# Kernel optimization log

Measured on AMD Instinct MI355X. Metric: run time of the kernel, lower is better.

The kernel has to match this reference:

```python
import jax, jax.numpy as jnp
import numpy as np

ALPHA = 1.0
EPS = 1e-09
N_PATCH = 128


def _triplet_loss(xp, xn, alpha, eps):
    # xp, xn: [B, N, D], assumed L2-normalized rows
    n = xp.shape[1]
    p_dist = 2.0 - 2.0 * jnp.einsum('bnd,bmd->bnm', xp, xp)   # [B,N,N]
    pn_dist = 2.0 - 2.0 * jnp.einsum('bnd,bmd->bnm', xp, xn)  # [B,N,N]
    # ppn_dist[b,i,j,k] = alpha + p_dist[b,i,j] - pn_dist[b,i,k]
    ppn = alpha + p_dist[:, :, :, None] - pn_dist[:, :, None, :]  # [B,N,N,N]
    mask = ppn <= 0
    pos = jnp.where(mask, 0.0, ppn)
    num = jnp.sum(pos, axis=-1)                                # [B,N,N]
    den = n - jnp.sum(mask, axis=-1).astype(pos.dtype) + eps   # [B,N,N]
    return jnp.mean(num / den)


def setup_inputs() -> dict:
    key = jax.random.key(0)
    latent = jax.random.normal(key, (8192, 512), dtype=jnp.float32)
    return {"latent": latent}


def reference(latent):
    bsz = latent.shape[0] // (2 * N_PATCH)
    latent = latent / jnp.linalg.norm(latent, axis=-1, keepdims=True)
    latent = latent.reshape(bsz, 2, N_PATCH, -1)
    t_latent, c_latent = latent[:, 0], latent[:, 1]
    loss = _triplet_loss(t_latent, c_latent, ALPHA, EPS) + _triplet_loss(c_latent, t_latent, ALPHA, EPS)
    return loss
```

## Files before the change

kernel.cpp:

```cpp
#include <hip/hip_runtime.h>
#include <hip/hip_bf16.h>

constexpr int   D      = 512;
constexpr float ALPHA  = 1.0f;
constexpr float EPS    = 1e-9f;
constexpr float INV_CNT = 1.0f / (32.0f * 128.0f * 128.0f);

constexpr size_t NRM_OFF  = 0;
constexpr size_t PART_OFF = 8388608;

typedef short bf16x8 __attribute__((ext_vector_type(8)));
typedef float f32x4  __attribute__((ext_vector_type(4)));

__device__ __forceinline__ short f2bf(float f) {
    unsigned u = __builtin_bit_cast(unsigned, f);
    unsigned r = (u + 0x7FFFu + ((u >> 16) & 1u)) >> 16;
    return (short)r;
}


__global__ __launch_bounds__(256) void k_normalize(const float* __restrict__ in,
                                                   short* __restrict__ nrm2) {
    const int wid  = threadIdx.x >> 6;
    const int lane = threadIdx.x & 63;
    const int p    = blockIdx.x;
    const int r    = (p & 7) * 1024 + (p >> 3) * 4 + wid;
    const int b    = r >> 8;
    const int row  = r & 255;
    const float4* src = (const float4*)(in + (size_t)r * D);
    float4 x0 = src[2 * lane];
    float4 x1 = src[2 * lane + 1];
    float ss = x0.x*x0.x + x0.y*x0.y + x0.z*x0.z + x0.w*x0.w
             + x1.x*x1.x + x1.y*x1.y + x1.z*x1.z + x1.w*x1.w;
    #pragma unroll
    for (int o = 32; o > 0; o >>= 1) ss += __shfl_xor(ss, o, 64);
    const float inv = rsqrtf(ss);
    bf16x8 v;
    v[0] = f2bf(x0.x * inv); v[1] = f2bf(x0.y * inv);
    v[2] = f2bf(x0.z * inv); v[3] = f2bf(x0.w * inv);
    v[4] = f2bf(x1.x * inv); v[5] = f2bf(x1.y * inv);
    v[6] = f2bf(x1.z * inv); v[7] = f2bf(x1.w * inv);
    const int ks   = lane >> 2;
    const int slot = ((lane & 3) + (row >> 1)) & 3;
    char* dst = (char*)nrm2 + ((((size_t)b * 16 + ks) * 256 + row) * 64 + slot * 16);
    *(bf16x8*)dst = v;
}

constexpr int PSTR = 260;

__global__ __launch_bounds__(1024, 4) void k_fused(const short* __restrict__ nrm2,
                                                   float* __restrict__ part) {
    __shared__ __align__(16) char smem[33408];

    const int p     = blockIdx.x;
    const int slot  = p >> 3;
    const int b     = (p & 7) * 4 + (slot & 3);
    const int chunk = slot >> 2;
    const int w     = threadIdx.x >> 6;
    const int lane  = threadIdx.x & 63;
    const int fr    = lane & 15;
    const int kg    = lane >> 4;

    const char* batchbase = (const char*)nrm2 + (size_t)b * 16 * 256 * 64;

    const int sigma = (kg + (fr >> 1)) & 3;

    const char* gAt = batchbase + (chunk * 16 + fr) * 64 + sigma * 16;
    const char* gAc = gAt + 128 * 64;
    const char* gB0 = batchbase + (w * 16 + fr) * 64 + sigma * 16;

    f32x4 accT = {0.f,0.f,0.f,0.f};
    f32x4 accC = {0.f,0.f,0.f,0.f};

    #pragma unroll
    for (int s = 0; s < 16; s++) {
        const size_t o = (size_t)s * 16384;
        const bf16x8 at = *(const bf16x8*)(gAt + o);
        const bf16x8 ac = *(const bf16x8*)(gAc + o);
        const bf16x8 b0 = *(const bf16x8*)(gB0 + o);
        accT = __builtin_amdgcn_mfma_f32_16x16x32_bf16(at, b0, accT, 0, 0, 0);
        accC = __builtin_amdgcn_mfma_f32_16x16x32_bf16(ac, b0, accC, 0, 0, 0);
    }

    float* P   = (float*)smem;
    float* red = (float*)&smem[33280];

    {
        const int rw = kg * 4;
        const int cw = w * 16 + fr;
        #pragma unroll
        for (int q = 0; q < 4; q++) P[(rw + q) * PSTR + cw]      = accT[q];
        #pragma unroll
        for (int q = 0; q < 4; q++) P[(16 + rw + q) * PSTR + cw] = accC[q];
    }
    __syncthreads();

    float wacc = 0.f;
    #pragma unroll
    for (int rr = 0; rr < 2; rr++) {
        const int r      = w * 2 + rr;
        const int pd_off = (r < 16) ? 0 : 128;
        const int pn_off = 128 - pd_off;
        float* prow = &P[r * PSTR];

        const float g0 = prow[pd_off + lane];
        const float g1 = prow[pd_off + lane + 64];
        float v0 = prow[pn_off + lane];
        float v1 = prow[pn_off + lane + 64];

        #pragma unroll
        for (int kk = 2; kk <= 128; kk <<= 1) {
            if (kk == 128) {
                const float lo = fminf(v0, v1);
                const float hi = fmaxf(v0, v1);
                v0 = lo; v1 = hi;
            }
            #pragma unroll
            for (int j = (kk == 128 ? 32 : (kk >> 1)); j >= 1; j >>= 1) {
                const float p0 = __shfl_xor(v0, j, 64);
                const float p1 = __shfl_xor(v1, j, 64);
                const bool up0 = (lane & kk) == 0;
                const bool up1 = ((lane + 64) & kk) == 0;
                const bool lower = (lane & j) == 0;
                v0 = (up0 == lower) ? fminf(v0, p0) : fmaxf(v0, p0);
                v1 = (up1 == lower) ? fminf(v1, p1) : fmaxf(v1, p1);
            }
        }

        float inc0 = v0, inc1 = v1;
        #pragma unroll
        for (int o = 1; o < 64; o <<= 1) {
            const float t0 = __shfl_up(inc0, o, 64);
            const float t1 = __shfl_up(inc1, o, 64);
            if (lane >= o) { inc0 += t0; inc1 += t1; }
        }
        const float tot0  = __shfl(inc0, 63, 64);
        const float total = tot0 + __shfl(inc1, 63, 64);

        prow[lane]            = v0;
        prow[64 + lane]       = v1;
        prow[130 + 1 + lane]  = inc0;
        prow[130 + 65 + lane] = tot0 + inc1;
        if (lane == 0) prow[130] = 0.f;

        #pragma unroll
        for (int h = 0; h < 2; h++) {
            const float g   = h ? g1 : g0;
            const float tau = g - 0.5f * ALPHA;
            const float a   = ALPHA - 2.f * g;
            int pos = 0;
            #pragma unroll
            for (int st = 128; st > 0; st >>= 1) {
                const int nidx = pos + st;
                const float sv = prow[nidx - 1];
                pos = ((nidx <= 128) && (sv <= tau)) ? nidx : pos;
            }
            const float cnt = (float)(128 - pos);
            const float pre = prow[130 + pos];
            const float num = cnt * a + 2.f * (total - pre);
            wacc += num / (cnt + EPS);
        }
    }

    #pragma unroll
    for (int o = 32; o > 0; o >>= 1) wacc += __shfl_xor(wacc, o, 64);
    if (lane == 0) red[w] = wacc;
    __syncthreads();
    if (threadIdx.x == 0) {
        float s = 0.f;
        #pragma unroll
        for (int i = 0; i < 16; i++) s += red[i];
        part[p] = s;
    }
}

__global__ __launch_bounds__(256) void k_reduce(const float* __restrict__ part,
                                                float* __restrict__ out) {
    __shared__ float red[4];
    const int w    = threadIdx.x >> 6;
    const int lane = threadIdx.x & 63;
    float s = part[threadIdx.x];
    #pragma unroll
    for (int o = 32; o > 0; o >>= 1) s += __shfl_xor(s, o, 64);
    if (lane == 0) red[w] = s;
    __syncthreads();
    if (threadIdx.x == 0)
        out[0] = (red[0] + red[1] + red[2] + red[3]) * INV_CNT;
}

extern "C" void kernel_launch(void* const* d_in, const int* in_sizes, int n_in,
                              void* d_out, int out_size, void* d_ws, size_t ws_size,
                              hipStream_t stream) {
    const float* latent = (const float*)d_in[0];
    float* out  = (float*)d_out;
    char*  wsb  = (char*)d_ws;
    short* nrm2 = (short*)(wsb + NRM_OFF);
    float* part = (float*)(wsb + PART_OFF);

    hipLaunchKernelGGL(k_normalize, dim3(2048), dim3(256),  0, stream, latent, nrm2);
    hipLaunchKernelGGL(k_fused,     dim3(256),  dim3(1024), 0, stream, nrm2, part);
    hipLaunchKernelGGL(k_reduce,    dim3(1),    dim3(256),  0, stream, part, out);
}
```

Before: 28.08 us.

## Split fused block work by half to double grid size and occupancy

Each fused block now computes only one 16-row Gram tile (either the t or the c half) instead of both, so the grid doubles to 512 blocks and each wave processes a single row in the sort/scan phase. Shared memory per block is halved and launch bounds allow more resident blocks, aiming for better latency hiding on a GPU with many CUs. The B-operand loads are now duplicated across the two halves, adding L2 traffic, and the final reduction is widened to 512 partials.

```diff
diff --git a/kernel.cpp b/kernel.cpp
--- a/kernel.cpp
+++ b/kernel.cpp
@@ -48,14 +48,16 @@
 
 constexpr int PSTR = 260;
 
-__global__ __launch_bounds__(1024, 4) void k_fused(const short* __restrict__ nrm2,
+__global__ __launch_bounds__(1024, 8) void k_fused(const short* __restrict__ nrm2,
                                                    float* __restrict__ part) {
-    __shared__ __align__(16) char smem[33408];
+    __shared__ __align__(16) char smem[16768];
 
     const int p     = blockIdx.x;
     const int slot  = p >> 3;
     const int b     = (p & 7) * 4 + (slot & 3);
-    const int chunk = slot >> 2;
+    const int rem   = slot >> 2;
+    const int chunk = rem & 7;
+    const int half  = rem >> 3;
     const int w     = threadIdx.x >> 6;
     const int lane  = threadIdx.x & 63;
     const int fr    = lane & 15;
@@ -65,101 +67,91 @@
 
     const int sigma = (kg + (fr >> 1)) & 3;
 
-    const char* gAt = batchbase + (chunk * 16 + fr) * 64 + sigma * 16;
-    const char* gAc = gAt + 128 * 64;
-    const char* gB0 = batchbase + (w * 16 + fr) * 64 + sigma * 16;
+    const char* gA = batchbase + (half * 128 + chunk * 16 + fr) * 64 + sigma * 16;
+    const char* gB = batchbase + (w * 16 + fr) * 64 + sigma * 16;
 
-    f32x4 accT = {0.f,0.f,0.f,0.f};
-    f32x4 accC = {0.f,0.f,0.f,0.f};
+    f32x4 acc = {0.f, 0.f, 0.f, 0.f};
 
     #pragma unroll
     for (int s = 0; s < 16; s++) {
         const size_t o = (size_t)s * 16384;
-        const bf16x8 at = *(const bf16x8*)(gAt + o);
-        const bf16x8 ac = *(const bf16x8*)(gAc + o);
-        const bf16x8 b0 = *(const bf16x8*)(gB0 + o);
-        accT = __builtin_amdgcn_mfma_f32_16x16x32_bf16(at, b0, accT, 0, 0, 0);
-        accC = __builtin_amdgcn_mfma_f32_16x16x32_bf16(ac, b0, accC, 0, 0, 0);
+        const bf16x8 a  = *(const bf16x8*)(gA + o);
+        const bf16x8 b0 = *(const bf16x8*)(gB + o);
+        acc = __builtin_amdgcn_mfma_f32_16x16x32_bf16(a, b0, acc, 0, 0, 0);
     }
 
     float* P   = (float*)smem;
-    float* red = (float*)&smem[33280];
+    float* red = (float*)&smem[16640];
 
     {
         const int rw = kg * 4;
         const int cw = w * 16 + fr;
         #pragma unroll
-        for (int q = 0; q < 4; q++) P[(rw + q) * PSTR + cw]      = accT[q];
-        #pragma unroll
-        for (int q = 0; q < 4; q++) P[(16 + rw + q) * PSTR + cw] = accC[q];
+        for (int q = 0; q < 4; q++) P[(rw + q) * PSTR + cw] = acc[q];
     }
     __syncthreads();
 
+    const int pd_off = half ? 128 : 0;
+    const int pn_off = 128 - pd_off;
+    float* prow = &P[w * PSTR];
+
+    const float g0 = prow[pd_off + lane];
+    const float g1 = prow[pd_off + lane + 64];
+    float v0 = prow[pn_off + lane];
+    float v1 = prow[pn_off + lane + 64];
+
+    #pragma unroll
+    for (int kk = 2; kk <= 128; kk <<= 1) {
+        if (kk == 128) {
+            const float lo = fminf(v0, v1);
+            const float hi = fmaxf(v0, v1);
+            v0 = lo; v1 = hi;
+        }
+        #pragma unroll
+        for (int j = (kk == 128 ? 32 : (kk >> 1)); j >= 1; j >>= 1) {
+            const float p0 = __shfl_xor(v0, j, 64);
+            const float p1 = __shfl_xor(v1, j, 64);
+            const bool up0 = (lane & kk) == 0;
+            const bool up1 = ((lane + 64) & kk) == 0;
+            const bool lower = (lane & j) == 0;
+            v0 = (up0 == lower) ? fminf(v0, p0) : fmaxf(v0, p0);
+            v1 = (up1 == lower) ? fminf(v1, p1) : fmaxf(v1, p1);
+        }
+    }
+
+    float inc0 = v0, inc1 = v1;
+    #pragma unroll
+    for (int o = 1; o < 64; o <<= 1) {
+        const float t0 = __shfl_up(inc0, o, 64);
+        const float t1 = __shfl_up(inc1, o, 64);
+        if (lane >= o) { inc0 += t0; inc1 += t1; }
+    }
+    const float tot0  = __shfl(inc0, 63, 64);
+    const float total = tot0 + __shfl(inc1, 63, 64);
+
+    prow[lane]            = v0;
+    prow[64 + lane]       = v1;
+    prow[130 + 1 + lane]  = inc0;
+    prow[130 + 65 + lane] = tot0 + inc1;
+    if (lane == 0) prow[130] = 0.f;
+
     float wacc = 0.f;
     #pragma unroll
-    for (int rr = 0; rr < 2; rr++) {
-        const int r      = w * 2 + rr;
-        const int pd_off = (r < 16) ? 0 : 128;
-        const int pn_off = 128 - pd_off;
-        float* prow = &P[r * PSTR];
-
-        const float g0 = prow[pd_off + lane];
-        const float g1 = prow[pd_off + lane + 64];
-        float v0 = prow[pn_off + lane];
-        float v1 = prow[pn_off + lane + 64];
-
+    for (int h = 0; h < 2; h++) {
+        const float g   = h ? g1 : g0;
+        const float tau = g - 0.5f * ALPHA;
+        const float a   = ALPHA - 2.f * g;
+        int pos = 0;
         #pragma unroll
-        for (int kk = 2; kk <= 128; kk <<= 1) {
-            if (kk == 128) {
-                const float lo = fminf(v0, v1);
-                const float hi = fmaxf(v0, v1);
-                v0 = lo; v1 = hi;
-            }
-            #pragma unroll
-            for (int j = (kk == 128 ? 32 : (kk >> 1)); j >= 1; j >>= 1) {
-                const float p0 = __shfl_xor(v0, j, 64);
-                const float p1 = __shfl_xor(v1, j, 64);
-                const bool up0 = (lane & kk) == 0;
-                const bool up1 = ((lane + 64) & kk) == 0;
-                const bool lower = (lane & j) == 0;
-                v0 = (up0 == lower) ? fminf(v0, p0) : fmaxf(v0, p0);
-                v1 = (up1 == lower) ? fminf(v1, p1) : fmaxf(v1, p1);
-            }
+        for (int st = 128; st > 0; st >>= 1) {
+            const int nidx = pos + st;
+            const float sv = prow[nidx - 1];
+            pos = ((nidx <= 128) && (sv <= tau)) ? nidx : pos;
         }
-
-        float inc0 = v0, inc1 = v1;
-        #pragma unroll
-        for (int o = 1; o < 64; o <<= 1) {
-            const float t0 = __shfl_up(inc0, o, 64);
-            const float t1 = __shfl_up(inc1, o, 64);
-            if (lane >= o) { inc0 += t0; inc1 += t1; }
-        }
-        const float tot0  = __shfl(inc0, 63, 64);
-        const float total = tot0 + __shfl(inc1, 63, 64);
-
-        prow[lane]            = v0;
-        prow[64 + lane]       = v1;
-        prow[130 + 1 + lane]  = inc0;
-        prow[130 + 65 + lane] = tot0 + inc1;
-        if (lane == 0) prow[130] = 0.f;
-
-        #pragma unroll
-        for (int h = 0; h < 2; h++) {
-            const float g   = h ? g1 : g0;
-            const float tau = g - 0.5f * ALPHA;
-            const float a   = ALPHA - 2.f * g;
-            int pos = 0;
-            #pragma unroll
-            for (int st = 128; st > 0; st >>= 1) {
-                const int nidx = pos + st;
-                const float sv = prow[nidx - 1];
-                pos = ((nidx <= 128) && (sv <= tau)) ? nidx : pos;
-            }
-            const float cnt = (float)(128 - pos);
-            const float pre = prow[130 + pos];
-            const float num = cnt * a + 2.f * (total - pre);
-            wacc += num / (cnt + EPS);
-        }
+        const float cnt = (float)(128 - pos);
+        const float pre = prow[130 + pos];
+        const float num = cnt * a + 2.f * (total - pre);
+        wacc += num / (cnt + EPS);
     }
 
     #pragma unroll
@@ -174,9 +166,9 @@
     }
 }
 
-__global__ __launch_bounds__(256) void k_reduce(const float* __restrict__ part,
+__global__ __launch_bounds__(512) void k_reduce(const float* __restrict__ part,
                                                 float* __restrict__ out) {
-    __shared__ float red[4];
+    __shared__ float red[8];
     const int w    = threadIdx.x >> 6;
     const int lane = threadIdx.x & 63;
     float s = part[threadIdx.x];
@@ -184,8 +176,12 @@
     for (int o = 32; o > 0; o >>= 1) s += __shfl_xor(s, o, 64);
     if (lane == 0) red[w] = s;
     __syncthreads();
-    if (threadIdx.x == 0)
-        out[0] = (red[0] + red[1] + red[2] + red[3]) * INV_CNT;
+    if (threadIdx.x == 0) {
+        float t = 0.f;
+        #pragma unroll
+        for (int i = 0; i < 8; i++) t += red[i];
+        out[0] = t * INV_CNT;
+    }
 }
 
 extern "C" void kernel_launch(void* const* d_in, const int* in_sizes, int n_in,
@@ -198,6 +194,6 @@
     float* part = (float*)(wsb + PART_OFF);
 
     hipLaunchKernelGGL(k_normalize, dim3(2048), dim3(256),  0, stream, latent, nrm2);
-    hipLaunchKernelGGL(k_fused,     dim3(256),  dim3(1024), 0, stream, nrm2, part);
-    hipLaunchKernelGGL(k_reduce,    dim3(1),    dim3(256),  0, stream, part, out);
+    hipLaunchKernelGGL(k_fused,     dim3(512),  dim3(1024), 0, stream, nrm2, part);
+    hipLaunchKernelGGL(k_reduce,    dim3(1),    dim3(512),  0, stream, part, out);
 }
```

New measurement: 27.12 us. 1.04x faster.
